# Kernel tuning notes

Measured on AMD Instinct MI355X. Metric: run time of the kernel, lower is better.

The kernel has to match this reference:

```python
import math
import jax, jax.numpy as jnp
import numpy as np

T = 4096
D_MODEL = 1024
NUM_HEADS = 16
HEAD_DIM = D_MODEL // NUM_HEADS


def setup_inputs() -> dict:
    key = jax.random.key(0)
    k_x, k_wqkv, k_wproj = jax.random.split(key, 3)
    # match eqx.nn.Linear init scale: U(-1/sqrt(in), 1/sqrt(in)); randn*small works too,
    # but keep magnitudes reasonable so softmax isn't saturated.
    s_in = 1.0 / math.sqrt(D_MODEL)
    x = jax.random.normal(k_x, (T, D_MODEL), dtype=jnp.float32)
    W_qkv = jax.random.normal(k_wqkv, (3 * D_MODEL, D_MODEL), dtype=jnp.float32) * s_in
    b_qkv = jnp.zeros((3 * D_MODEL,), dtype=jnp.float32)
    W_proj = jax.random.normal(k_wproj, (D_MODEL, D_MODEL), dtype=jnp.float32) * s_in
    b_proj = jnp.zeros((D_MODEL,), dtype=jnp.float32)
    return {"x": x, "W_qkv": W_qkv, "b_qkv": b_qkv, "W_proj": W_proj, "b_proj": b_proj}


def reference(x, W_qkv, b_qkv, W_proj, b_proj):
    T_, C = x.shape  # (seq, d_model)
    H, hd = NUM_HEADS, HEAD_DIM
    # c_attn: eqx Linear computes W @ x + b per token -> x @ W.T + b
    qkv = x @ W_qkv.T + b_qkv  # (T, 3C)
    q, k, v = jnp.split(qkv, 3, axis=1)
    # (T, C) -> (H, T, hd)
    q = q.reshape(T_, H, hd).swapaxes(0, 1)
    k = k.reshape(T_, H, hd).swapaxes(0, 1)
    v = v.reshape(T_, H, hd).swapaxes(0, 1)
    scores = jnp.einsum("htd,hsd->hts", q, k) / math.sqrt(hd)  # (H, T, T)
    causal = jnp.tril(jnp.ones((T_, T_), dtype=bool))
    scores = jnp.where(causal, scores, -jnp.inf)
    attn = jax.nn.softmax(scores, axis=-1)
    y = jnp.einsum("hts,hsd->htd", attn, v)  # (H, T, hd)
    y = y.swapaxes(0, 1).reshape(T_, C)
    y = y @ W_proj.T + b_proj
    return y
```

## Files before the change

### kernel.cpp

```cpp
#include <hip/hip_runtime.h>
#include <math.h>
#include <string.h>

#define T_SEQ 4096
#define DM 1024
#define NH 16
#define HD 64

typedef short s8v __attribute__((ext_vector_type(8)));
typedef float f4v __attribute__((ext_vector_type(4)));

__device__ inline unsigned short f2bf(float f) {
    unsigned u; memcpy(&u, &f, 4);
    u = u + 0x7fffu + ((u >> 16) & 1u);
    return (unsigned short)(u >> 16);
}

__device__ inline float bf2f(unsigned short s) {
    unsigned u = (unsigned)s << 16;
    float f; memcpy(&f, &u, 4);
    return f;
}

__device__ inline float exp2fn(float x) {
#if __has_builtin(__builtin_amdgcn_exp2f)
    return __builtin_amdgcn_exp2f(x);
#else
    return exp2f(x);
#endif
}

__device__ inline void gld_lds16(const void* g, void* l) {
    __builtin_amdgcn_global_load_lds(
        (const __attribute__((address_space(1))) void*)g,
        (__attribute__((address_space(3))) void*)l, 16, 0, 0);
}

__global__ __launch_bounds__(256)
void cvt3(const float* __restrict__ i0, unsigned short* __restrict__ o0, int n0,
          const float* __restrict__ i1, unsigned short* __restrict__ o1, int n1,
          const float* __restrict__ i2, unsigned short* __restrict__ o2, int n2) {
    int i = blockIdx.x * 256 + threadIdx.x;
    const float* in; unsigned short* out; int j;
    if (i < n0)           { in = i0; out = o0; j = i; }
    else if (i < n0 + n1) { in = i1; out = o1; j = i - n0; }
    else if (i < n0 + n1 + n2) { in = i2; out = o2; j = i - n0 - n1; }
    else return;
    const float4* p = (const float4*)(in + (size_t)j * 8);
    float4 a = p[0], b = p[1];
    unsigned short o[8] = {f2bf(a.x), f2bf(a.y), f2bf(a.z), f2bf(a.w),
                           f2bf(b.x), f2bf(b.y), f2bf(b.z), f2bf(b.w)};
    uint4 pk; memcpy(&pk, o, 16);
    *(uint4*)(out + (size_t)j * 8) = pk;
}

template<int MODE, int TM, int TN, int WR, int WC>
__global__ __launch_bounds__(WR * WC * 64, 1)
void gemm_tile(const unsigned short* __restrict__ A, const unsigned short* __restrict__ B,
               const float* __restrict__ bias, void* __restrict__ Cout,
               unsigned short* __restrict__ qbuf, unsigned short* __restrict__ kbuf2,
               unsigned short* __restrict__ vT,
               int M, int N, int K, int nbx, int patchw, int patchh) {
    constexpr int W  = WR * WC;
    constexpr int MF = TM / WR / 16;
    constexpr int NF = TN / WC / 16;
    constexpr int NGA = TM / 16, NGB = TN / 16, NG = NGA + NGB;
    __shared__ __align__(16) short As[2][TM * 32];
    __shared__ __align__(16) short Bs[2][TN * 32];
    const int tid = threadIdx.x;
    const int w = tid >> 6, lane = tid & 63;
    const int wr = w / WC, wc = w % WC;
    const int l15 = lane & 15, quad = lane >> 4;

    const int bl = blockIdx.x;
    const int xcd = bl & 7, ii = bl >> 3;
    const int pxn = nbx / patchw;
    const int bx = (xcd % pxn) * patchw + ii % patchw;
    const int by = (xcd / pxn) * patchh + ii / patchw;
    const int m0 = by * TM, n0 = bx * TN;

    f4v acc[MF][NF];
    #pragma unroll
    for (int i = 0; i < MF; ++i)
        #pragma unroll
        for (int j = 0; j < NF; ++j) acc[i][j] = (f4v){0.f, 0.f, 0.f, 0.f};

    auto stage = [&](int buf, int k0) {
        for (int g = w; g < NG; g += W) {
            const unsigned short* src;
            short* dst;
            if (g < NGA) {
                src = A + (size_t)(m0 + g * 16 + l15) * K + quad * 8 + k0;
                dst = &As[buf][g * 512];
            } else {
                src = B + (size_t)(n0 + (g - NGA) * 16 + l15) * K + quad * 8 + k0;
                dst = &Bs[buf][(g - NGA) * 512];
            }
            gld_lds16(src, dst);
        }
    };
    auto compute = [&](int buf) {
        s8v af[MF], bfr[NF];
        #pragma unroll
        for (int i = 0; i < MF; ++i)
            af[i] = *(const s8v*)&As[buf][((wr * MF + i) * 64 + lane) * 8];
        #pragma unroll
        for (int j = 0; j < NF; ++j)
            bfr[j] = *(const s8v*)&Bs[buf][((wc * NF + j) * 64 + lane) * 8];
        #pragma unroll
        for (int i = 0; i < MF; ++i)
            #pragma unroll
            for (int j = 0; j < NF; ++j)
                acc[i][j] = __builtin_amdgcn_mfma_f32_16x16x32_bf16(af[i], bfr[j], acc[i][j], 0, 0, 0);
    };

    stage(0, 0);
    __syncthreads();
    for (int k0 = 0; k0 < K; k0 += 64) {
        stage(1, k0 + 32);
        compute(0);
        __syncthreads();
        if (k0 + 64 < K) stage(0, k0 + 64);
        compute(1);
        __syncthreads();
    }

    float bj[NF];
    #pragma unroll
    for (int j = 0; j < NF; ++j) bj[j] = bias[n0 + wc * (TN / WC) + j * 16 + l15];

    if (MODE == 2) {
        #pragma unroll
        for (int j = 0; j < NF; ++j) {
            const int ccol = n0 + wc * (TN / WC) + j * 16;
            if (ccol >= 2 * DM) {
                const int hh = (ccol - 2 * DM) >> 6;
                const int ob = (ccol & 63) >> 4;
                #pragma unroll
                for (int i = 0; i < MF; ++i) {
                    const int tile = (m0 + wr * (TM / WR)) / 64 + (i >> 2);
                    const int it = i & 3;
                    unsigned short o[4];
                    #pragma unroll
                    for (int rg = 0; rg < 4; ++rg) o[rg] = f2bf(acc[i][j][rg] + bj[j]);
                    unsigned long long pk; memcpy(&pk, o, 8);
                    size_t off = (size_t)hh * 262144 + (size_t)tile * 4096
                               + (size_t)((ob * 2 + (it >> 1)) * 64 + lane) * 8 + (it & 1) * 4;
                    *(unsigned long long*)&vT[off] = pk;
                }
            } else {
                unsigned short* dst = (ccol < DM) ? qbuf : kbuf2;
                const int col = (ccol < DM) ? (ccol + l15) : (ccol - DM + l15);
                #pragma unroll
                for (int i = 0; i < MF; ++i) {
                    #pragma unroll
                    for (int rg = 0; rg < 4; ++rg) {
                        int row = m0 + wr * (TM / WR) + i * 16 + quad * 4 + rg;
                        dst[(size_t)row * DM + col] = f2bf(acc[i][j][rg] + bj[j]);
                    }
                }
            }
        }
    } else {
        #pragma unroll
        for (int i = 0; i < MF; ++i) {
            #pragma unroll
            for (int rg = 0; rg < 4; ++rg) {
                int row = m0 + wr * (TM / WR) + i * 16 + quad * 4 + rg;
                #pragma unroll
                for (int j = 0; j < NF; ++j) {
                    int col = n0 + wc * (TN / WC) + j * 16 + l15;
                    ((float*)Cout)[(size_t)row * N + col] = acc[i][j][rg] + bj[j];
                }
            }
        }
    }
}

__device__ __forceinline__ void soft_step(f4v* st, bool diag, int qloc, int quad,
                                          float& lr, s8v& pf0, s8v& pf1) {
    const float C2  = 0.1803368851f;
    const float MC2 = 12.0f * 0.1803368851f;
    float sv[4][4];
    #pragma unroll
    for (int kb = 0; kb < 4; ++kb)
        #pragma unroll
        for (int rg = 0; rg < 4; ++rg) {
            float s = st[kb][rg];
            if (diag && (kb * 16 + quad * 4 + rg > qloc)) s = -3.0e38f;
            float t = exp2fn(fmaf(s, C2, -MC2));
            sv[kb][rg] = t;
            lr += t;
        }
    int pk[4][2];
    #pragma unroll
    for (int kb = 0; kb < 4; ++kb) {
        unsigned u0 = __float_as_uint(sv[kb][0]) + 0x8000u;
        unsigned u1 = __float_as_uint(sv[kb][1]) + 0x8000u;
        unsigned u2 = __float_as_uint(sv[kb][2]) + 0x8000u;
        unsigned u3 = __float_as_uint(sv[kb][3]) + 0x8000u;
        pk[kb][0] = (int)__builtin_amdgcn_perm(u1, u0, 0x07060302);
        pk[kb][1] = (int)__builtin_amdgcn_perm(u3, u2, 0x07060302);
    }
    int4 a = {pk[0][0], pk[0][1], pk[1][0], pk[1][1]};
    int4 b = {pk[2][0], pk[2][1], pk[3][0], pk[3][1]};
    memcpy(&pf0, &a, 16);
    memcpy(&pf1, &b, 16);
}

__global__ __launch_bounds__(512, 4)
void attn_mfma2p(const unsigned short* __restrict__ qb,
                 const unsigned short* __restrict__ kbf,
                 const unsigned short* __restrict__ vT,
                 unsigned short* __restrict__ y0,
                 unsigned short* __restrict__ y1,
                 float* __restrict__ lsum) {
    const int b = blockIdx.x;
    const int par = b >> 8;
    const int idx = b & 255;
    const int h = idx & 15, a = idx >> 4;
    const int tid = threadIdx.x;
    const int w = tid >> 6, lane = tid & 63;
    const int quad = lane >> 4, l15 = lane & 15;
    const int cq = h * HD;
    unsigned short* ypar = par ? y1 : y0;
    float* lpar = lsum + ((size_t)par * NH + h) * T_SEQ;
    const unsigned short* vbase = vT + (size_t)h * 262144;

    __shared__ short KB[2][4096];
    __shared__ short VTs[2][4096];
    __shared__ short QB[8192];

    const bool lo = (w < 4);
    const int qloc = (w & 3) * 16 + l15;

    for (int ph = 0; ph < 2; ++ph) {
        const int qt = ph ? (31 - a) : a;
        const int q0 = qt * 128;
        const int nk = qt + 1;
        const int kt0 = par * 64;

        __syncthreads();
        #pragma unroll
        for (int rr = 0; rr < 2; ++rr) {
            int ch = rr * 512 + tid;
            int qg = ch >> 7, hf = (ch >> 6) & 1, ln = ch & 63;
            gld_lds16(qb + (size_t)(q0 + qg * 16 + (ln & 15)) * DM + cq + hf * 32 + ((ln >> 4) << 3),
                      &QB[(ch & ~63) * 8]);
        }
        {
            int ch = tid;
            int blk = ch >> 7, hf = (ch >> 6) & 1, ln = ch & 63;
            gld_lds16(kbf + (size_t)(kt0 + blk * 16 + (ln & 15)) * DM + cq + hf * 32 + ((ln >> 4) << 3),
                      &KB[0][(ch & ~63) * 8]);
            gld_lds16(vbase + (size_t)(kt0 >> 6) * 4096 + (size_t)ch * 8,
                      &VTs[0][(ch & ~63) * 8]);
        }
        __syncthreads();

        s8v qf[2];
        #pragma unroll
        for (int hf = 0; hf < 2; ++hf)
            qf[hf] = *(const s8v*)&QB[(((w * 2 + hf) * 64) + lane) * 8];

        f4v O[4];
        #pragma unroll
        for (int ob = 0; ob < 4; ++ob) O[ob] = (f4v){0.f, 0.f, 0.f, 0.f};
        float lr = 0.f;

        for (int i = 0; i < nk; ++i) {
            const int kt = par + 2 * i;
            const int p = i & 1;
            const bool diag = lo ? (kt == 2 * qt) : (kt == 2 * qt + 1);
            const bool skip = lo && (kt == 2 * qt + 1);
            if (i < nk - 1) {
                const int k1 = kt0 + (i + 1) * 128;
                int ch = tid;
                int blk = ch >> 7, hf = (ch >> 6) & 1, ln = ch & 63;
                gld_lds16(kbf + (size_t)(k1 + blk * 16 + (ln & 15)) * DM + cq
                              + hf * 32 + ((ln >> 4) << 3),
                          &KB[p ^ 1][(ch & ~63) * 8]);
                gld_lds16(vbase + (size_t)(k1 >> 6) * 4096 + (size_t)ch * 8,
                          &VTs[p ^ 1][(ch & ~63) * 8]);
            }

            if (!skip) {
                f4v st[4];
                #pragma unroll
                for (int kb = 0; kb < 4; ++kb) {
                    s8v k0f = *(const s8v*)&KB[p][((kb * 2 + 0) * 64 + lane) * 8];
                    s8v k1f = *(const s8v*)&KB[p][((kb * 2 + 1) * 64 + lane) * 8];
                    f4v c = (f4v){0.f, 0.f, 0.f, 0.f};
                    c = __builtin_amdgcn_mfma_f32_16x16x32_bf16(k0f, qf[0], c, 0, 0, 0);
                    c = __builtin_amdgcn_mfma_f32_16x16x32_bf16(k1f, qf[1], c, 0, 0, 0);
                    st[kb] = c;
                }
                s8v pf0, pf1;
                soft_step(st, diag, qloc, quad, lr, pf0, pf1);
                #pragma unroll
                for (int ob = 0; ob < 4; ++ob) {
                    s8v v0f = *(const s8v*)&VTs[p][((ob * 2 + 0) * 64 + lane) * 8];
                    s8v v1f = *(const s8v*)&VTs[p][((ob * 2 + 1) * 64 + lane) * 8];
                    O[ob] = __builtin_amdgcn_mfma_f32_16x16x32_bf16(v0f, pf0, O[ob], 0, 0, 0);
                    O[ob] = __builtin_amdgcn_mfma_f32_16x16x32_bf16(v1f, pf1, O[ob], 0, 0, 0);
                }
            }
            __syncthreads();
        }

        lr += __shfl_xor(lr, 16); lr += __shfl_xor(lr, 32);
        const int qrow = q0 + w * 16 + l15;
        const size_t ybase = (size_t)qrow * DM + cq;
        #pragma unroll
        for (int ob = 0; ob < 4; ++ob) {
            unsigned short o[4];
            #pragma unroll
            for (int rg = 0; rg < 4; ++rg) o[rg] = f2bf(O[ob][rg]);
            unsigned long long pk; memcpy(&pk, o, 8);
            *(unsigned long long*)&ypar[ybase + ob * 16 + quad * 4] = pk;
        }
        if (quad == 0) lpar[qrow] = lr;
    }
}

__global__ __launch_bounds__(256)
void attn_combine2(const unsigned short* __restrict__ y0,
                   const unsigned short* __restrict__ y1,
                   const float* __restrict__ lsum,
                   unsigned short* __restrict__ yout) {
    int i = blockIdx.x * 256 + threadIdx.x;
    int t = i >> 7, d8 = i & 127;
    int h = d8 >> 3;
    float l = lsum[(size_t)h * T_SEQ + t]
            + lsum[((size_t)NH + h) * T_SEQ + t];
    float inv = 1.f / l;
    size_t off = (size_t)t * DM + d8 * 8;
    uint4 ua = *(const uint4*)(y0 + off);
    uint4 ub = *(const uint4*)(y1 + off);
    const unsigned short* pa = (const unsigned short*)&ua;
    const unsigned short* pb = (const unsigned short*)&ub;
    unsigned short o[8];
    #pragma unroll
    for (int k = 0; k < 8; ++k)
        o[k] = f2bf((bf2f(pa[k]) + bf2f(pb[k])) * inv);
    uint4 pk; memcpy(&pk, o, 16);
    *(uint4*)(yout + off) = pk;
}

extern "C" void kernel_launch(void* const* d_in, const int* in_sizes, int n_in,
                              void* d_out, int out_size, void* d_ws, size_t ws_size,
                              hipStream_t stream) {
    const float* x     = (const float*)d_in[0];
    const float* Wqkv  = (const float*)d_in[1];
    const float* bqkv  = (const float*)d_in[2];
    const float* Wproj = (const float*)d_in[3];
    const float* bproj = (const float*)d_in[4];
    float* out = (float*)d_out;

    char* ws = (char*)d_ws;
    unsigned short* qbuf  = (unsigned short*)(ws);
    unsigned short* kbuf  = (unsigned short*)(ws + ( 8u << 20));
    unsigned short* vTb   = (unsigned short*)(ws + (16u << 20));
    unsigned short* yattb = (unsigned short*)(ws + (24u << 20));
    unsigned short* wprjb = (unsigned short*)(ws + (32u << 20));
    float*          lsum  = (float*)         (ws + (34u << 20));
    unsigned short* xb    = (unsigned short*)(ws + (35u << 20));
    unsigned short* wqkvb = (unsigned short*)(ws + (43u << 20));
    unsigned short* y0p   = (unsigned short*)(ws + (35u << 20));
    unsigned short* y1p   = (unsigned short*)(ws + (43u << 20));

    {
        int n0 = T_SEQ * DM / 8, n1 = 3 * DM * DM / 8, n2 = DM * DM / 8;
        cvt3<<<dim3((n0 + n1 + n2 + 255) / 256), dim3(256), 0, stream>>>(
            x, xb, n0, Wqkv, wqkvb, n1, Wproj, wprjb, n2);
    }
    gemm_tile<2, 256, 192, 2, 4><<<dim3(256), dim3(512), 0, stream>>>(
        xb, wqkvb, bqkv, nullptr, qbuf, kbuf, vTb, T_SEQ, 3 * DM, DM, 16, 8, 4);
    attn_mfma2p<<<dim3(512), dim3(512), 0, stream>>>(qbuf, kbuf, vTb, y0p, y1p, lsum);
    attn_combine2<<<dim3(T_SEQ * DM / 8 / 256), dim3(256), 0, stream>>>(y0p, y1p, lsum, yattb);
    gemm_tile<0, 128, 128, 2, 2><<<dim3(256), dim3(256), 0, stream>>>(
        yattb, wprjb, bproj, out, nullptr, nullptr, nullptr, T_SEQ, DM, DM, 8, 4, 8);
}
```

Before: 212.2 us.

## Fuse all stages into one cooperative persistent kernel with grid syncs

Replaces the five separate launches (convert, QKV GEMM, split attention, combine, projection GEMM) with a single cooperative kernel of 256 blocks of 512 threads that separates stages with grid.sync. The attention stage drops the two-way key split and the combine pass, so each block walks the full causal key range and normalizes its own output. The projection GEMM now uses 8 waves per block instead of 4. This removes launch gaps and the combine kernel's memory traffic, but attention parallelism halves (256 blocks instead of 512, at one block per CU), and every stage is forced to 512 threads with 1-block occupancy.

```diff
diff --git a/kernel.cpp b/kernel.cpp
--- a/kernel.cpp
+++ b/kernel.cpp
@@ -1,6 +1,9 @@
 #include <hip/hip_runtime.h>
+#include <hip/hip_cooperative_groups.h>
 #include <math.h>
 #include <string.h>
+
+namespace cg = cooperative_groups;
 
 #define T_SEQ 4096
 #define DM 1024
@@ -36,37 +39,20 @@
         (__attribute__((address_space(3))) void*)l, 16, 0, 0);
 }
 
-__global__ __launch_bounds__(256)
-void cvt3(const float* __restrict__ i0, unsigned short* __restrict__ o0, int n0,
-          const float* __restrict__ i1, unsigned short* __restrict__ o1, int n1,
-          const float* __restrict__ i2, unsigned short* __restrict__ o2, int n2) {
-    int i = blockIdx.x * 256 + threadIdx.x;
-    const float* in; unsigned short* out; int j;
-    if (i < n0)           { in = i0; out = o0; j = i; }
-    else if (i < n0 + n1) { in = i1; out = o1; j = i - n0; }
-    else if (i < n0 + n1 + n2) { in = i2; out = o2; j = i - n0 - n1; }
-    else return;
-    const float4* p = (const float4*)(in + (size_t)j * 8);
-    float4 a = p[0], b = p[1];
-    unsigned short o[8] = {f2bf(a.x), f2bf(a.y), f2bf(a.z), f2bf(a.w),
-                           f2bf(b.x), f2bf(b.y), f2bf(b.z), f2bf(b.w)};
-    uint4 pk; memcpy(&pk, o, 16);
-    *(uint4*)(out + (size_t)j * 8) = pk;
-}
 
 template<int MODE, int TM, int TN, int WR, int WC>
-__global__ __launch_bounds__(WR * WC * 64, 1)
-void gemm_tile(const unsigned short* __restrict__ A, const unsigned short* __restrict__ B,
-               const float* __restrict__ bias, void* __restrict__ Cout,
-               unsigned short* __restrict__ qbuf, unsigned short* __restrict__ kbuf2,
-               unsigned short* __restrict__ vT,
-               int M, int N, int K, int nbx, int patchw, int patchh) {
+__device__ void gemm_body(char* smem_,
+                          const unsigned short* __restrict__ A, const unsigned short* __restrict__ B,
+                          const float* __restrict__ bias, void* __restrict__ Cout,
+                          unsigned short* __restrict__ qbuf, unsigned short* __restrict__ kbuf2,
+                          unsigned short* __restrict__ vT,
+                          int M, int N, int K, int nbx, int patchw, int patchh) {
     constexpr int W  = WR * WC;
     constexpr int MF = TM / WR / 16;
     constexpr int NF = TN / WC / 16;
     constexpr int NGA = TM / 16, NGB = TN / 16, NG = NGA + NGB;
-    __shared__ __align__(16) short As[2][TM * 32];
-    __shared__ __align__(16) short Bs[2][TN * 32];
+    short* AsB = (short*)smem_;
+    short* BsB = (short*)smem_ + 2 * TM * 32;
     const int tid = threadIdx.x;
     const int w = tid >> 6, lane = tid & 63;
     const int wr = w / WC, wc = w % WC;
@@ -86,27 +72,26 @@
         for (int j = 0; j < NF; ++j) acc[i][j] = (f4v){0.f, 0.f, 0.f, 0.f};
 
     auto stage = [&](int buf, int k0) {
+        short* As = AsB + buf * TM * 32;
+        short* Bs = BsB + buf * TN * 32;
         for (int g = w; g < NG; g += W) {
-            const unsigned short* src;
-            short* dst;
-            if (g < NGA) {
-                src = A + (size_t)(m0 + g * 16 + l15) * K + quad * 8 + k0;
-                dst = &As[buf][g * 512];
-            } else {
-                src = B + (size_t)(n0 + (g - NGA) * 16 + l15) * K + quad * 8 + k0;
-                dst = &Bs[buf][(g - NGA) * 512];
-            }
-            gld_lds16(src, dst);
+            if (g < NGA)
+                gld_lds16(A + (size_t)(m0 + g * 16 + l15) * K + quad * 8 + k0, &As[g * 512]);
+            else
+                gld_lds16(B + (size_t)(n0 + (g - NGA) * 16 + l15) * K + quad * 8 + k0,
+                          &Bs[(g - NGA) * 512]);
         }
     };
     auto compute = [&](int buf) {
+        short* As = AsB + buf * TM * 32;
+        short* Bs = BsB + buf * TN * 32;
         s8v af[MF], bfr[NF];
         #pragma unroll
         for (int i = 0; i < MF; ++i)
-            af[i] = *(const s8v*)&As[buf][((wr * MF + i) * 64 + lane) * 8];
+            af[i] = *(const s8v*)&As[((wr * MF + i) * 64 + lane) * 8];
         #pragma unroll
         for (int j = 0; j < NF; ++j)
-            bfr[j] = *(const s8v*)&Bs[buf][((wc * NF + j) * 64 + lane) * 8];
+            bfr[j] = *(const s8v*)&Bs[((wc * NF + j) * 64 + lane) * 8];
         #pragma unroll
         for (int i = 0; i < MF; ++i)
             #pragma unroll
@@ -208,37 +193,28 @@
     memcpy(&pf1, &b, 16);
 }
 
-__global__ __launch_bounds__(512, 4)
-void attn_mfma2p(const unsigned short* __restrict__ qb,
-                 const unsigned short* __restrict__ kbf,
-                 const unsigned short* __restrict__ vT,
-                 unsigned short* __restrict__ y0,
-                 unsigned short* __restrict__ y1,
-                 float* __restrict__ lsum) {
+__device__ void attn_body(char* smem_,
+                          const unsigned short* __restrict__ qb,
+                          const unsigned short* __restrict__ kbf,
+                          const unsigned short* __restrict__ vT,
+                          unsigned short* __restrict__ yout) {
+    short (*KB)[4096]  = (short(*)[4096])smem_;
+    short (*VTs)[4096] = (short(*)[4096])(smem_ + 16384);
+    short* QB          = (short*)(smem_ + 32768);
     const int b = blockIdx.x;
-    const int par = b >> 8;
-    const int idx = b & 255;
-    const int h = idx & 15, a = idx >> 4;
+    const int h = b & 15, a = b >> 4;
     const int tid = threadIdx.x;
     const int w = tid >> 6, lane = tid & 63;
     const int quad = lane >> 4, l15 = lane & 15;
     const int cq = h * HD;
-    unsigned short* ypar = par ? y1 : y0;
-    float* lpar = lsum + ((size_t)par * NH + h) * T_SEQ;
     const unsigned short* vbase = vT + (size_t)h * 262144;
-
-    __shared__ short KB[2][4096];
-    __shared__ short VTs[2][4096];
-    __shared__ short QB[8192];
-
     const bool lo = (w < 4);
     const int qloc = (w & 3) * 16 + l15;
 
     for (int ph = 0; ph < 2; ++ph) {
         const int qt = ph ? (31 - a) : a;
         const int q0 = qt * 128;
-        const int nk = qt + 1;
-        const int kt0 = par * 64;
+        const int nk = 2 * qt + 2;
 
         __syncthreads();
         #pragma unroll
@@ -251,10 +227,9 @@
         {
             int ch = tid;
             int blk = ch >> 7, hf = (ch >> 6) & 1, ln = ch & 63;
-            gld_lds16(kbf + (size_t)(kt0 + blk * 16 + (ln & 15)) * DM + cq + hf * 32 + ((ln >> 4) << 3),
+            gld_lds16(kbf + (size_t)(blk * 16 + (ln & 15)) * DM + cq + hf * 32 + ((ln >> 4) << 3),
                       &KB[0][(ch & ~63) * 8]);
-            gld_lds16(vbase + (size_t)(kt0 >> 6) * 4096 + (size_t)ch * 8,
-                      &VTs[0][(ch & ~63) * 8]);
+            gld_lds16(vbase + (size_t)ch * 8, &VTs[0][(ch & ~63) * 8]);
         }
         __syncthreads();
 
@@ -269,12 +244,12 @@
         float lr = 0.f;
 
         for (int i = 0; i < nk; ++i) {
-            const int kt = par + 2 * i;
+            const int kt = i;
             const int p = i & 1;
             const bool diag = lo ? (kt == 2 * qt) : (kt == 2 * qt + 1);
             const bool skip = lo && (kt == 2 * qt + 1);
             if (i < nk - 1) {
-                const int k1 = kt0 + (i + 1) * 128;
+                const int k1 = (i + 1) * 64;
                 int ch = tid;
                 int blk = ch >> 7, hf = (ch >> 6) & 1, ln = ch & 63;
                 gld_lds16(kbf + (size_t)(k1 + blk * 16 + (ln & 15)) * DM + cq
@@ -309,42 +284,64 @@
         }
 
         lr += __shfl_xor(lr, 16); lr += __shfl_xor(lr, 32);
+        const float inv = 1.f / lr;
         const int qrow = q0 + w * 16 + l15;
         const size_t ybase = (size_t)qrow * DM + cq;
         #pragma unroll
         for (int ob = 0; ob < 4; ++ob) {
             unsigned short o[4];
             #pragma unroll
-            for (int rg = 0; rg < 4; ++rg) o[rg] = f2bf(O[ob][rg]);
+            for (int rg = 0; rg < 4; ++rg) o[rg] = f2bf(O[ob][rg] * inv);
             unsigned long long pk; memcpy(&pk, o, 8);
-            *(unsigned long long*)&ypar[ybase + ob * 16 + quad * 4] = pk;
-        }
-        if (quad == 0) lpar[qrow] = lr;
-    }
-}
-
-__global__ __launch_bounds__(256)
-void attn_combine2(const unsigned short* __restrict__ y0,
-                   const unsigned short* __restrict__ y1,
-                   const float* __restrict__ lsum,
-                   unsigned short* __restrict__ yout) {
-    int i = blockIdx.x * 256 + threadIdx.x;
-    int t = i >> 7, d8 = i & 127;
-    int h = d8 >> 3;
-    float l = lsum[(size_t)h * T_SEQ + t]
-            + lsum[((size_t)NH + h) * T_SEQ + t];
-    float inv = 1.f / l;
-    size_t off = (size_t)t * DM + d8 * 8;
-    uint4 ua = *(const uint4*)(y0 + off);
-    uint4 ub = *(const uint4*)(y1 + off);
-    const unsigned short* pa = (const unsigned short*)&ua;
-    const unsigned short* pb = (const unsigned short*)&ub;
-    unsigned short o[8];
-    #pragma unroll
-    for (int k = 0; k < 8; ++k)
-        o[k] = f2bf((bf2f(pa[k]) + bf2f(pb[k])) * inv);
-    uint4 pk; memcpy(&pk, o, 16);
-    *(uint4*)(yout + off) = pk;
+            *(unsigned long long*)&yout[ybase + ob * 16 + quad * 4] = pk;
+        }
+    }
+}
+
+__global__ __launch_bounds__(512, 1)
+void mega(const float* __restrict__ x, const float* __restrict__ Wqkv,
+          const float* __restrict__ bqkv, const float* __restrict__ Wproj,
+          const float* __restrict__ bproj, float* __restrict__ out,
+          unsigned short* __restrict__ xb, unsigned short* __restrict__ wqkvb,
+          unsigned short* __restrict__ wprjb, unsigned short* __restrict__ qbuf,
+          unsigned short* __restrict__ kbuf, unsigned short* __restrict__ vTb,
+          unsigned short* __restrict__ yattb) {
+    cg::grid_group grid = cg::this_grid();
+    __shared__ __align__(16) char smem[57344];
+
+    {
+        const int n0 = T_SEQ * DM / 8, n1 = 3 * DM * DM / 8, n2 = DM * DM / 8;
+        const int ntot = n0 + n1 + n2;
+        for (int i = blockIdx.x * 512 + threadIdx.x; i < ntot; i += 256 * 512) {
+            const float* in; unsigned short* o8; int j;
+            if (i < n0)           { in = x;     o8 = xb;    j = i; }
+            else if (i < n0 + n1) { in = Wqkv;  o8 = wqkvb; j = i - n0; }
+            else                  { in = Wproj; o8 = wprjb; j = i - n0 - n1; }
+            const float4* p = (const float4*)(in + (size_t)j * 8);
+            float4 va = p[0], vb = p[1];
+            unsigned short o[8] = {f2bf(va.x), f2bf(va.y), f2bf(va.z), f2bf(va.w),
+                                   f2bf(vb.x), f2bf(vb.y), f2bf(vb.z), f2bf(vb.w)};
+            uint4 pk; memcpy(&pk, o, 16);
+            *(uint4*)(o8 + (size_t)j * 8) = pk;
+        }
+    }
+    __threadfence();
+    grid.sync();
+    __threadfence();
+
+    gemm_body<2, 256, 192, 2, 4>(smem, xb, wqkvb, bqkv, nullptr,
+                                 qbuf, kbuf, vTb, T_SEQ, 3 * DM, DM, 16, 8, 4);
+    __threadfence();
+    grid.sync();
+    __threadfence();
+
+    attn_body(smem, qbuf, kbuf, vTb, yattb);
+    __threadfence();
+    grid.sync();
+    __threadfence();
+
+    gemm_body<0, 128, 128, 2, 4>(smem, yattb, wprjb, bproj, out,
+                                 nullptr, nullptr, nullptr, T_SEQ, DM, DM, 8, 4, 8);
 }
 
 extern "C" void kernel_launch(void* const* d_in, const int* in_sizes, int n_in,
@@ -363,21 +360,13 @@
     unsigned short* vTb   = (unsigned short*)(ws + (16u << 20));
     unsigned short* yattb = (unsigned short*)(ws + (24u << 20));
     unsigned short* wprjb = (unsigned short*)(ws + (32u << 20));
-    float*          lsum  = (float*)         (ws + (34u << 20));
     unsigned short* xb    = (unsigned short*)(ws + (35u << 20));
     unsigned short* wqkvb = (unsigned short*)(ws + (43u << 20));
-    unsigned short* y0p   = (unsigned short*)(ws + (35u << 20));
-    unsigned short* y1p   = (unsigned short*)(ws + (43u << 20));
-
-    {
-        int n0 = T_SEQ * DM / 8, n1 = 3 * DM * DM / 8, n2 = DM * DM / 8;
-        cvt3<<<dim3((n0 + n1 + n2 + 255) / 256), dim3(256), 0, stream>>>(
-            x, xb, n0, Wqkv, wqkvb, n1, Wproj, wprjb, n2);
-    }
-    gemm_tile<2, 256, 192, 2, 4><<<dim3(256), dim3(512), 0, stream>>>(
-        xb, wqkvb, bqkv, nullptr, qbuf, kbuf, vTb, T_SEQ, 3 * DM, DM, 16, 8, 4);
-    attn_mfma2p<<<dim3(512), dim3(512), 0, stream>>>(qbuf, kbuf, vTb, y0p, y1p, lsum);
-    attn_combine2<<<dim3(T_SEQ * DM / 8 / 256), dim3(256), 0, stream>>>(y0p, y1p, lsum, yattb);
-    gemm_tile<0, 128, 128, 2, 2><<<dim3(256), dim3(256), 0, stream>>>(
-        yattb, wprjb, bproj, out, nullptr, nullptr, nullptr, T_SEQ, DM, DM, 8, 4, 8);
-}
+
+    void* args[] = {
+        (void*)&x, (void*)&Wqkv, (void*)&bqkv, (void*)&Wproj, (void*)&bproj,
+        (void*)&out, (void*)&xb, (void*)&wqkvb, (void*)&wprjb,
+        (void*)&qbuf, (void*)&kbuf, (void*)&vTb, (void*)&yattb
+    };
+    hipLaunchCooperativeKernel((void*)mega, dim3(256), dim3(512), args, 0, stream);
+}
```

Result: slower. 568.9 us (+168.0%).
